# Optimization experiments

Hardware: AMD Instinct MI355X
Metric: run time of the kernel (lower is better)

## Reference

```python
import jax, jax.numpy as jnp
import numpy as np

CONTEXT_LENGTHS = [1, 3, 5, 7]
PADS = [(f - 1) // 2 for f in CONTEXT_LENGTHS]  # p(f) for odd f
B, H, L, DK = 2, 8, 1024, 64
C = H * DK  # conv channels = d_k * n_heads


def _conv1d(x, w, b, pad):
    # x: (b, C, L), w: (C, C, f), b: (C,) -- torch Conv1d semantics
    y = jax.lax.conv_general_dilated(
        x, w, window_strides=(1,), padding=[(pad, pad)],
        dimension_numbers=("NCH", "OIH", "NCH"))
    return y + b[None, :, None]


def _plane(a, w, b, pad, out_len):
    # Faithful to: conv(a.reshape(b, h*d_k, -1)).reshape(b, h, -1, d_k)[:, :, :out_len, :]
    bsz, h, l, d = a.shape
    y = _conv1d(a.reshape(bsz, h * d, l), w, b, pad)
    return y.reshape(bsz, h, -1, d)[:, :, :out_len, :]


def setup_inputs() -> dict:
    key = jax.random.key(0)
    ks = jax.random.split(key, 12)
    inp = {
        "Q": jax.random.normal(ks[0], (B, H, L, DK), jnp.float32),
        "K": jax.random.normal(ks[1], (B, H, L, DK), jnp.float32),
        "V": jax.random.normal(ks[2], (B, H, L, DK), jnp.float32),
        # causal mask: True = masked
        "attn_mask": jnp.broadcast_to(
            jnp.triu(jnp.ones((L, L), jnp.bool_), k=1), (B, H, L, L)),
    }
    for i, f in enumerate(CONTEXT_LENGTHS):
        scale = 1.0 / np.sqrt(C * f)
        inp[f"conv_w{i}"] = jax.random.normal(ks[3 + i], (C, C, f), jnp.float32) * scale
        inp[f"conv_b{i}"] = jax.random.normal(ks[7 + i], (C,), jnp.float32) * scale
    return inp


def reference(Q, K, V, attn_mask,
              conv_w0, conv_b0, conv_w1, conv_b1,
              conv_w2, conv_b2, conv_w3, conv_b3):
    ws = [conv_w0, conv_w1, conv_w2, conv_w3]
    bs = [conv_b0, conv_b1, conv_b2, conv_b3]
    b, h, l, d_k = Q.shape
    l_k = K.shape[2]
    p = len(CONTEXT_LENGTHS)
    Q_l = [_plane(Q, ws[i], bs[i], PADS[i], l) for i in range(p)]
    K_l = [_plane(K, ws[i], bs[i], PADS[i], l_k) for i in range(p)]
    # replicate torch.cat(dim=0).reshape(b, h, p, l, d) exactly (row-major)
    Q_p = jnp.concatenate(Q_l, axis=0).reshape(b, h, p, l, d_k)
    K_p = jnp.concatenate(K_l, axis=0).reshape(b, h, p, l_k, d_k)
    scores = jnp.einsum("bhpqd,bhpkd->bhpqk", Q_p, K_p) / np.sqrt(d_k).astype(np.float32)
    scores = jnp.where(attn_mask[:, :, None, :, :], jnp.float32(-1e9), scores)
    attn = jax.nn.softmax(scores, axis=-1)
    attn = jnp.max(attn, axis=2)  # max over planes -> (b,h,q,k)
    context = jnp.einsum("bhqk,bhkd->bhqd", attn, V)
    return (context, attn)
```

## Files before the change

### kernel.cpp

```cpp
#include <hip/hip_runtime.h>
#include <math.h>

#define C_CH 512
#define L_SEQ 1024
#define DK 64
#define NP 4
#define SC2 0.1803368801111f

typedef __attribute__((ext_vector_type(8))) short short8;
typedef __attribute__((ext_vector_type(4))) float f32x4;

__device__ __forceinline__ unsigned short f2bf(float f) {
    union { float f; unsigned u; } v; v.f = f;
    unsigned u = v.u;
    u += 0x7FFFu + ((u >> 16) & 1u);
    return (unsigned short)(u >> 16);
}

__device__ __forceinline__ void unpack_tile128(int G, int& qt8, int& kt) {
    int cum = 0;
    for (int q8 = 7; q8 >= 0; q8--) {
        int c = 2 * q8 + 2;
        if (G < cum + c) { qt8 = q8; kt = G - cum; return; }
        cum += c;
    }
    qt8 = 0; kt = 0;
}

__global__ __launch_bounds__(256)
void prep_w_kernel(const float* __restrict__ w0, const float* __restrict__ w1,
                   const float* __restrict__ w2, const float* __restrict__ w3,
                   unsigned short* __restrict__ Wb) {
    int tg = blockIdx.y;
    int plane, t;
    if (tg < 1)      { plane = 0; t = tg; }
    else if (tg < 4) { plane = 1; t = tg - 1; }
    else if (tg < 9) { plane = 2; t = tg - 4; }
    else             { plane = 3; t = tg - 9; }
    const float* W = (plane == 0) ? w0 : (plane == 1) ? w1 : (plane == 2) ? w2 : w3;
    const int f = (plane == 0) ? 1 : (plane == 1) ? 3 : (plane == 2) ? 5 : 7;

    int co = blockIdx.x * 32 + (threadIdx.x >> 3);
    int c8 = threadIdx.x & 7;
    for (int it = 0; it < 8; it++) {
        int ci = c8 * 8 + it * 64;
        unsigned short o[8];
#pragma unroll
        for (int jj = 0; jj < 8; jj++)
            o[jj] = f2bf(W[(size_t)(co * C_CH + ci + jj) * f + t]);
        *(short8*)&Wb[((size_t)tg * C_CH + co) * C_CH + ci] = *(short8*)o;
    }
}

__global__ __launch_bounds__(256)
void prep_x_kernel(const float* __restrict__ Qin, const float* __restrict__ Kin,
                   unsigned short* __restrict__ Xt) {
    int tb = blockIdx.z;
    int tensor = tb >> 1, b = tb & 1;
    const float* X = (tensor ? Kin : Qin) + (size_t)b * C_CH * L_SEQ;
    unsigned short* O = Xt + (size_t)tb * 1032 * C_CH;

    int pos0 = blockIdx.x * 64;
    int ci0  = blockIdx.y * 64;
    int tid = threadIdx.x;

    __shared__ float tile[64][65];
    int tx = tid & 15, ty = tid >> 4;
#pragma unroll
    for (int rr = 0; rr < 4; rr++) {
        int ci_l = ty + rr * 16;
        float4 v = *(const float4*)&X[(size_t)(ci0 + ci_l) * L_SEQ + pos0 + tx * 4];
        tile[tx * 4 + 0][ci_l] = v.x;
        tile[tx * 4 + 1][ci_l] = v.y;
        tile[tx * 4 + 2][ci_l] = v.z;
        tile[tx * 4 + 3][ci_l] = v.w;
    }
    __syncthreads();
#pragma unroll
    for (int pp = 0; pp < 2; pp++) {
        int pos_l = (tid >> 3) + pp * 32;
        int cg = (tid & 7) * 8;
        unsigned short o[8];
#pragma unroll
        for (int jj = 0; jj < 8; jj++) o[jj] = f2bf(tile[pos_l][cg + jj]);
        *(short8*)&O[(size_t)(pos0 + pos_l + 4) * C_CH + ci0 + cg] = *(short8*)o;
    }
    if (blockIdx.x == 0) {
        int r = tid >> 6, cc = tid & 63;
        O[(size_t)r * C_CH + ci0 + cc] = 0;
    }
    if (blockIdx.x == 15) {
        int r = tid >> 6, cc = tid & 63;
        O[(size_t)(1028 + r) * C_CH + ci0 + cc] = 0;
    }
}

__global__ __launch_bounds__(256)
void conv_mfma_kernel(const unsigned short* __restrict__ Xt,
                      const unsigned short* __restrict__ Wb,
                      const float* __restrict__ b0, const float* __restrict__ b1,
                      const float* __restrict__ b2, const float* __restrict__ b3,
                      unsigned short* __restrict__ Qp, unsigned short* __restrict__ Kp) {
    const int fs[4]   = {1, 3, 5, 7};
    const int toff[4] = {0, 1, 4, 9};
    int id = blockIdx.x;
    int plane, rel;
    if (id < 128)      { plane = 0; rel = id; }
    else if (id < 256) { plane = 1; rel = id - 128; }
    else if (id < 384) { plane = 3; rel = id - 256; }
    else               { plane = 2; rel = id - 384; }
    int co0  = (rel & 3) * 128;
    int pos0 = ((rel >> 2) & 7) * 128;
    int tb   = rel >> 5;
    int tensor = tb >> 1, b = tb & 1;
    const int f   = fs[plane];
    const int pad = (f - 1) >> 1;
    const int n   = f * 16;
    const float* bias = (plane == 0) ? b0 : (plane == 1) ? b1 : (plane == 2) ? b2 : b3;
    unsigned short* Out = tensor ? Kp : Qp;
    const unsigned short* Xbase = Xt + (size_t)tb * 1032 * C_CH;

    __shared__ __align__(16) unsigned short As[2][4096];
    __shared__ __align__(16) unsigned short Bs[2][4096];

    int tid  = threadIdx.x;
    int w    = tid >> 6;
    int lane = tid & 63;
    int l15  = lane & 15;
    int quad = lane >> 4;
    int wm = (w & 1) * 64;
    int wn = (w >> 1) * 64;
    int rowL = tid >> 2;
    int cS   = tid & 3;

    int woff[2];
#pragma unroll
    for (int rep = 0; rep < 2; rep++) {
        int r = rowL + rep * 64;
        int line = r >> 1;
        int sl = (((r & 1) << 2) | cS) ^ (line & 7);
        woff[rep] = line * 64 + sl * 8;
    }
    int aoff[4], boff[4];
#pragma unroll
    for (int mi = 0; mi < 4; mi++) {
        int r = wm + mi * 16 + l15;
        int line = r >> 1;
        aoff[mi] = line * 64 + ((((r & 1) << 2) | quad) ^ (line & 7)) * 8;
        int r2 = wn + mi * 16 + l15;
        int line2 = r2 >> 1;
        boff[mi] = line2 * 64 + ((((r2 & 1) << 2) | quad) ^ (line2 & 7)) * 8;
    }

    f32x4 acc[4][4];
#pragma unroll
    for (int mi = 0; mi < 4; mi++)
#pragma unroll
        for (int ni = 0; ni < 4; ni++) acc[mi][ni] = (f32x4){0.f, 0.f, 0.f, 0.f};

    short8 pA[2], pB[2];
    {
        const unsigned short* Wsl = Wb + ((size_t)toff[plane] * C_CH + co0) * C_CH;
        const unsigned short* Xsl = Xbase + (size_t)(pos0 - pad + 4) * C_CH;
#pragma unroll
        for (int rep = 0; rep < 2; rep++) {
            int r = rowL + rep * 64;
            pA[rep] = *(const short8*)&Wsl[(size_t)r * C_CH + cS * 8];
            pB[rep] = *(const short8*)&Xsl[(size_t)r * C_CH + cS * 8];
        }
    }

    for (int it = 0; it < n; it++) {
        int cur = it & 1;
        *(short8*)&As[cur][woff[0]] = pA[0];
        *(short8*)&As[cur][woff[1]] = pA[1];
        *(short8*)&Bs[cur][woff[0]] = pB[0];
        *(short8*)&Bs[cur][woff[1]] = pB[1];
        __syncthreads();

        if (it + 1 < n) {
            int t = (it + 1) >> 4, cc = (it + 1) & 15;
            const unsigned short* Wsl =
                Wb + ((size_t)(toff[plane] + t) * C_CH + co0) * C_CH + cc * 32;
            const unsigned short* Xsl =
                Xbase + (size_t)(pos0 + t - pad + 4) * C_CH + cc * 32;
#pragma unroll
            for (int rep = 0; rep < 2; rep++) {
                int r = rowL + rep * 64;
                pA[rep] = *(const short8*)&Wsl[(size_t)r * C_CH + cS * 8];
                pB[rep] = *(const short8*)&Xsl[(size_t)r * C_CH + cS * 8];
            }
        }

        short8 af[4], bf[4];
#pragma unroll
        for (int mi = 0; mi < 4; mi++) af[mi] = *(const short8*)&As[cur][aoff[mi]];
#pragma unroll
        for (int ni = 0; ni < 4; ni++) bf[ni] = *(const short8*)&Bs[cur][boff[ni]];
#pragma unroll
        for (int mi = 0; mi < 4; mi++)
#pragma unroll
            for (int ni = 0; ni < 4; ni++)
                acc[mi][ni] = __builtin_amdgcn_mfma_f32_16x16x32_bf16(
                    af[mi], bf[ni], acc[mi][ni], 0, 0, 0);
    }

#pragma unroll
    for (int mi = 0; mi < 4; mi++)
#pragma unroll
        for (int r = 0; r < 4; r++) {
            int co = co0 + wm + mi * 16 + quad * 4 + r;
            int h = co >> 6, cl = co & 63;
            float bv = bias[co];
            size_t sbase = (size_t)((b * 8 + h) * NP + plane) * L_SEQ * DK;
#pragma unroll
            for (int ni = 0; ni < 4; ni++) {
                int pos = pos0 + wn + ni * 16 + l15;
                int l = cl * 16 + (pos >> 6);
                int d = pos & 63;
                Out[sbase + (size_t)l * DK + d] = f2bf(acc[mi][ni][r] + bv);
            }
        }
}

__global__ __launch_bounds__(512)
void attn_stats_kernel(const unsigned short* __restrict__ Qb,
                       const unsigned short* __restrict__ Kb,
                       float* __restrict__ pl) {
    int qt8, kt;
    unpack_tile128(blockIdx.x, qt8, kt);
    int bh = blockIdx.y;
    int tid = threadIdx.x;
    int w = tid >> 6, lane = tid & 63, l15 = lane & 15, quad = lane >> 4;
    int q0 = qt8 * 128, k0 = kt * 64;
    int qrow0 = q0 + w * 16;

    if (qrow0 + 15 < k0) return;

    int b2 = bh >> 3, h2 = bh & 7;
    int plane  = b2 * 2 + (h2 >> 2);
    int b_orig = (h2 >> 1) & 1;
    int h_base = (h2 & 1) * 4;

    float l[NP][4];
#pragma unroll
    for (int p = 0; p < NP; p++)
        for (int r = 0; r < 4; r++) l[p][r] = 0.f;

#pragma unroll
    for (int p = 0; p < NP; p++) {
        size_t slice = (size_t)((b_orig * 8 + h_base + p) * NP + plane);
        const unsigned short* kb = Kb + slice * L_SEQ * DK;
        const unsigned short* qrow =
            Qb + (slice * L_SEQ + (size_t)(qrow0 + l15)) * DK + quad * 8;
        short8 qa0 = *(const short8*)(qrow);
        short8 qa1 = *(const short8*)(qrow + 32);

        f32x4 c[4];
#pragma unroll
        for (int s = 0; s < 4; s++) {
            const unsigned short* kr = kb + (size_t)(k0 + s * 16 + l15) * DK + quad * 8;
            short8 kb0 = *(const short8*)(kr);
            short8 kb1 = *(const short8*)(kr + 32);
            f32x4 acc = {0.f, 0.f, 0.f, 0.f};
            acc = __builtin_amdgcn_mfma_f32_16x16x32_bf16(qa0, kb0, acc, 0, 0, 0);
            acc = __builtin_amdgcn_mfma_f32_16x16x32_bf16(qa1, kb1, acc, 0, 0, 0);
            c[s] = acc;
        }
#pragma unroll
        for (int r = 0; r < 4; r++) {
            int qg = qrow0 + quad * 4 + r;
#pragma unroll
            for (int s = 0; s < 4; s++) {
                float x = c[s][r] * SC2;
                if (k0 + s * 16 + l15 > qg) x = -1e30f;
                l[p][r] += exp2f(x);
            }
        }
    }

    int qt64 = qt8 * 2 + (w >> 2);
    size_t base = ((size_t)(bh * 16 + qt64) * 16 + kt) * 256;
#pragma unroll
    for (int p = 0; p < NP; p++)
#pragma unroll
        for (int r = 0; r < 4; r++) {
            float ll = l[p][r];
            ll += __shfl_xor(ll, 1);
            ll += __shfl_xor(ll, 2);
            ll += __shfl_xor(ll, 4);
            ll += __shfl_xor(ll, 8);
            if (l15 == 0)
                pl[base + p * 64 + ((w & 3) * 16 + quad * 4 + r)] = ll;
        }
}

__global__ __launch_bounds__(256)
void attn_combine_kernel(const float* __restrict__ pl,
                         float* __restrict__ fstats,
                         float* __restrict__ out_attn) {
    int qt = blockIdx.x, bh = blockIdx.y;
    int tid = threadIdx.x;
    size_t sb = (size_t)(bh * 16 + qt) * 16 * 256;

    float l = 0.f;
    for (int kt = 0; kt <= qt; kt++)
        l += pl[sb + (size_t)kt * 256 + tid];
    fstats[(size_t)(bh * 16 + qt) * 256 + tid] = __log2f(l);

    int r = tid >> 2;
    float4 z = make_float4(0.f, 0.f, 0.f, 0.f);
    int kz = (qt + 1) * 64;
    size_t abase = ((size_t)bh * L_SEQ + qt * 64 + r) * L_SEQ;
    for (int k = kz + (tid & 3) * 4; k < L_SEQ; k += 16)
        *(float4*)&out_attn[abase + k] = z;
}

__global__ __launch_bounds__(512)
void attn_apply_kernel(const unsigned short* __restrict__ Qb,
                       const unsigned short* __restrict__ Kb,
                       const float* __restrict__ fstats,
                       float* __restrict__ out_attn) {
    int qt8, kt;
    unpack_tile128(blockIdx.x, qt8, kt);
    int bh = blockIdx.y;
    int tid = threadIdx.x;
    int w = tid >> 6, lane = tid & 63, l15 = lane & 15, quad = lane >> 4;
    int q0 = qt8 * 128, k0 = kt * 64;
    int qrow0 = q0 + w * 16;

    __shared__ float zsm[512];
    {
        int p = tid >> 7, row = tid & 127;
        int qt64 = qt8 * 2 + (row >> 6);
        zsm[tid] = fstats[(size_t)(bh * 16 + qt64) * 256 + p * 64 + (row & 63)];
    }
    __syncthreads();

    if (qrow0 + 15 < k0) {
#pragma unroll
        for (int s = 0; s < 4; s++)
#pragma unroll
            for (int r = 0; r < 4; r++) {
                int qg = qrow0 + quad * 4 + r;
                out_attn[((size_t)bh * L_SEQ + qg) * L_SEQ + k0 + s * 16 + l15] = 0.f;
            }
        return;
    }

    int b2 = bh >> 3, h2 = bh & 7;
    int plane  = b2 * 2 + (h2 >> 2);
    int b_orig = (h2 >> 1) & 1;
    int h_base = (h2 & 1) * 4;

    float run[4][4];
#pragma unroll
    for (int s = 0; s < 4; s++)
        for (int r = 0; r < 4; r++) run[s][r] = -1e30f;

#pragma unroll
    for (int p = 0; p < NP; p++) {
        size_t slice = (size_t)((b_orig * 8 + h_base + p) * NP + plane);
        const unsigned short* kb = Kb + slice * L_SEQ * DK;
        const unsigned short* qrow =
            Qb + (slice * L_SEQ + (size_t)(qrow0 + l15)) * DK + quad * 8;
        short8 qa0 = *(const short8*)(qrow);
        short8 qa1 = *(const short8*)(qrow + 32);

        f32x4 c[4];
#pragma unroll
        for (int s = 0; s < 4; s++) {
            const unsigned short* kr = kb + (size_t)(k0 + s * 16 + l15) * DK + quad * 8;
            short8 kb0 = *(const short8*)(kr);
            short8 kb1 = *(const short8*)(kr + 32);
            f32x4 acc = {0.f, 0.f, 0.f, 0.f};
            acc = __builtin_amdgcn_mfma_f32_16x16x32_bf16(qa0, kb0, acc, 0, 0, 0);
            acc = __builtin_amdgcn_mfma_f32_16x16x32_bf16(qa1, kb1, acc, 0, 0, 0);
            c[s] = acc;
        }
#pragma unroll
        for (int r = 0; r < 4; r++) {
            float zp = zsm[p * 128 + (w * 16 + quad * 4 + r)];
#pragma unroll
            for (int s = 0; s < 4; s++)
                run[s][r] = fmaxf(run[s][r], c[s][r] * SC2 - zp);
        }
    }

#pragma unroll
    for (int s = 0; s < 4; s++)
#pragma unroll
        for (int r = 0; r < 4; r++) {
            int qg = qrow0 + quad * 4 + r;
            int kg = k0 + s * 16 + l15;
            float a = (kg > qg) ? 0.f : exp2f(run[s][r]);
            out_attn[((size_t)bh * L_SEQ + qg) * L_SEQ + kg] = a;
        }
}

__global__ __launch_bounds__(512)
void ctx_gemm_kernel(const float* __restrict__ attn, const float* __restrict__ V,
                     float* __restrict__ out_ctx) {
    int qt = 15 - blockIdx.x;
    int bh = blockIdx.y;
    int tid = threadIdx.x;
    int w = tid >> 6, lane = tid & 63, l15 = lane & 15, quad = lane >> 4;
    int q0 = qt * 64;
    int nk = (qt + 1) * 64;
    int wq = (w & 3) * 16;
    int ds0 = (w >> 2) * 2;

    __shared__ __align__(16) unsigned short vts[64 * 136];

    const float* Arow = attn + ((size_t)bh * L_SEQ + q0 + wq + l15) * L_SEQ;
    const float* Vb = V + (size_t)bh * L_SEQ * DK;

    f32x4 acc[2];
    acc[0] = (f32x4){0.f, 0.f, 0.f, 0.f};
    acc[1] = (f32x4){0.f, 0.f, 0.f, 0.f};

    for (int c0 = 0; c0 < nk; c0 += 128) {
        int rem = min(128, nk - c0);
        __syncthreads();
        {
            int kl = tid >> 2, db = (tid & 3) * 16;
            if (kl < rem) {
                const float* vr = Vb + (size_t)(c0 + kl) * DK + db;
                float vv[16];
                *(float4*)&vv[0]  = *(const float4*)(vr);
                *(float4*)&vv[4]  = *(const float4*)(vr + 4);
                *(float4*)&vv[8]  = *(const float4*)(vr + 8);
                *(float4*)&vv[12] = *(const float4*)(vr + 12);
#pragma unroll
                for (int jj = 0; jj < 16; jj++)
                    vts[(db + jj) * 136 + kl] = f2bf(vv[jj]);
            }
        }
        __syncthreads();

        int nss = rem >> 5;
        for (int ss = 0; ss < nss; ss++) {
            int kk = c0 + ss * 32 + quad * 8;
            float4 a0 = *(const float4*)&Arow[kk];
            float4 a1 = *(const float4*)&Arow[kk + 4];
            unsigned short af[8];
            af[0] = f2bf(a0.x); af[1] = f2bf(a0.y); af[2] = f2bf(a0.z); af[3] = f2bf(a0.w);
            af[4] = f2bf(a1.x); af[5] = f2bf(a1.y); af[6] = f2bf(a1.z); af[7] = f2bf(a1.w);
            short8 afv = *(short8*)af;
#pragma unroll
            for (int t = 0; t < 2; t++) {
                short8 bf = *(const short8*)&vts[((ds0 + t) * 16 + l15) * 136 +
                                                 ss * 32 + quad * 8];
                acc[t] = __builtin_amdgcn_mfma_f32_16x16x32_bf16(afv, bf, acc[t], 0, 0, 0);
            }
        }
    }

#pragma unroll
    for (int t = 0; t < 2; t++)
#pragma unroll
        for (int r = 0; r < 4; r++) {
            int qg = q0 + wq + quad * 4 + r;
            out_ctx[((size_t)bh * L_SEQ + qg) * DK + (ds0 + t) * 16 + l15] = acc[t][r];
        }
}

extern "C" void kernel_launch(void* const* d_in, const int* in_sizes, int n_in,
                              void* d_out, int out_size, void* d_ws, size_t ws_size,
                              hipStream_t stream) {
    const float* Q  = (const float*)d_in[0];
    const float* K  = (const float*)d_in[1];
    const float* V  = (const float*)d_in[2];
    const float* w0 = (const float*)d_in[4];
    const float* b0 = (const float*)d_in[5];
    const float* w1 = (const float*)d_in[6];
    const float* b1 = (const float*)d_in[7];
    const float* w2 = (const float*)d_in[8];
    const float* b2 = (const float*)d_in[9];
    const float* w3 = (const float*)d_in[10];
    const float* b3 = (const float*)d_in[11];

    char* ws = (char*)d_ws;
    unsigned short* Wb = (unsigned short*)(ws);
    unsigned short* Xt = (unsigned short*)(ws + 8388608);
    unsigned short* Qp = (unsigned short*)(ws + 12615680);
    unsigned short* Kp = (unsigned short*)(ws + 21004288);
    float* pl     = (float*)(ws);
    float* fstats = (float*)(ws + 4194304);

    float* out_ctx  = (float*)d_out;
    float* out_attn = out_ctx + 1048576;

    prep_w_kernel<<<dim3(16, 16), 256, 0, stream>>>(w0, w1, w2, w3, Wb);
    prep_x_kernel<<<dim3(16, 8, 4), 256, 0, stream>>>(Q, K, Xt);
    conv_mfma_kernel<<<dim3(512), 256, 0, stream>>>(Xt, Wb, b0, b1, b2, b3, Qp, Kp);
    attn_stats_kernel<<<dim3(72, 16), 512, 0, stream>>>(Qp, Kp, pl);
    attn_combine_kernel<<<dim3(16, 16), 256, 0, stream>>>(pl, fstats, out_attn);
    attn_apply_kernel<<<dim3(72, 16), 512, 0, stream>>>(Qp, Kp, fstats, out_attn);
    ctx_gemm_kernel<<<dim3(16, 16), 512, 0, stream>>>(out_attn, V, out_ctx);
}
```

Measured before the change: 374.0 us.

## Retile conv, fold combine into apply, split-K the context GEMM with reduction

```diff
diff --git a/kernel.cpp b/kernel.cpp
--- a/kernel.cpp
+++ b/kernel.cpp
@@ -25,6 +25,22 @@
         cum += c;
     }
     qt8 = 0; kt = 0;
+}
+
+__device__ __forceinline__ void unpack_group(int G, int& qt, int& kt0, int& kt1,
+                                             int& j, int& ng) {
+    int q = 15, cum = 0, jj = 0;
+    for (; q >= 0; q--) {
+        int g = (q + 4) >> 2;
+        if (G < cum + g) { jj = G - cum; break; }
+        cum += g;
+    }
+    qt = q;
+    ng = (q + 4) >> 2;
+    j = jj;
+    int n = q + 1;
+    kt0 = (jj * n) / ng;
+    kt1 = ((jj + 1) * n) / ng;
 }
 
 __global__ __launch_bounds__(256)
@@ -104,14 +120,11 @@
     const int fs[4]   = {1, 3, 5, 7};
     const int toff[4] = {0, 1, 4, 9};
     int id = blockIdx.x;
-    int plane, rel;
-    if (id < 128)      { plane = 0; rel = id; }
-    else if (id < 256) { plane = 1; rel = id - 128; }
-    else if (id < 384) { plane = 3; rel = id - 256; }
-    else               { plane = 2; rel = id - 384; }
+    int plane = (id < 256) ? 0 : (id < 512) ? 1 : (id < 768) ? 3 : 2;
+    int rel = id & 255;
     int co0  = (rel & 3) * 128;
-    int pos0 = ((rel >> 2) & 7) * 128;
-    int tb   = rel >> 5;
+    int pos0 = ((rel >> 2) & 15) * 64;
+    int tb   = rel >> 6;
     int tensor = tb >> 1, b = tb & 1;
     const int f   = fs[plane];
     const int pad = (f - 1) >> 1;
@@ -121,7 +134,7 @@
     const unsigned short* Xbase = Xt + (size_t)tb * 1032 * C_CH;
 
     __shared__ __align__(16) unsigned short As[2][4096];
-    __shared__ __align__(16) unsigned short Bs[2][4096];
+    __shared__ __align__(16) unsigned short Bs[2][2048];
 
     int tid  = threadIdx.x;
     int w    = tid >> 6;
@@ -129,53 +142,54 @@
     int l15  = lane & 15;
     int quad = lane >> 4;
     int wm = (w & 1) * 64;
-    int wn = (w >> 1) * 64;
-    int rowL = tid >> 2;
-    int cS   = tid & 3;
-
-    int woff[2];
+    int wn = (w >> 1) * 32;
+
+    int rA0 = tid >> 2, sA = tid & 3;
+    int woffA[2], woffB;
 #pragma unroll
     for (int rep = 0; rep < 2; rep++) {
-        int r = rowL + rep * 64;
+        int r = rA0 + rep * 64;
         int line = r >> 1;
-        int sl = (((r & 1) << 2) | cS) ^ (line & 7);
-        woff[rep] = line * 64 + sl * 8;
-    }
-    int aoff[4], boff[4];
+        woffA[rep] = line * 64 + (((((r & 1) << 2) | sA)) ^ (line & 7)) * 8;
+    }
+    {
+        int line = rA0 >> 1;
+        woffB = line * 64 + (((((rA0 & 1) << 2) | sA)) ^ (line & 7)) * 8;
+    }
+    int aoff[4], boff[2];
 #pragma unroll
     for (int mi = 0; mi < 4; mi++) {
         int r = wm + mi * 16 + l15;
         int line = r >> 1;
         aoff[mi] = line * 64 + ((((r & 1) << 2) | quad) ^ (line & 7)) * 8;
-        int r2 = wn + mi * 16 + l15;
-        int line2 = r2 >> 1;
-        boff[mi] = line2 * 64 + ((((r2 & 1) << 2) | quad) ^ (line2 & 7)) * 8;
-    }
-
-    f32x4 acc[4][4];
+    }
+#pragma unroll
+    for (int ni = 0; ni < 2; ni++) {
+        int r = wn + ni * 16 + l15;
+        int line = r >> 1;
+        boff[ni] = line * 64 + ((((r & 1) << 2) | quad) ^ (line & 7)) * 8;
+    }
+
+    f32x4 acc[4][2];
 #pragma unroll
     for (int mi = 0; mi < 4; mi++)
 #pragma unroll
-        for (int ni = 0; ni < 4; ni++) acc[mi][ni] = (f32x4){0.f, 0.f, 0.f, 0.f};
-
-    short8 pA[2], pB[2];
+        for (int ni = 0; ni < 2; ni++) acc[mi][ni] = (f32x4){0.f, 0.f, 0.f, 0.f};
+
+    short8 pA[2], pB;
     {
         const unsigned short* Wsl = Wb + ((size_t)toff[plane] * C_CH + co0) * C_CH;
         const unsigned short* Xsl = Xbase + (size_t)(pos0 - pad + 4) * C_CH;
-#pragma unroll
-        for (int rep = 0; rep < 2; rep++) {
-            int r = rowL + rep * 64;
-            pA[rep] = *(const short8*)&Wsl[(size_t)r * C_CH + cS * 8];
-            pB[rep] = *(const short8*)&Xsl[(size_t)r * C_CH + cS * 8];
-        }
+        pA[0] = *(const short8*)&Wsl[(size_t)rA0 * C_CH + sA * 8];
+        pA[1] = *(const short8*)&Wsl[(size_t)(rA0 + 64) * C_CH + sA * 8];
+        pB    = *(const short8*)&Xsl[(size_t)rA0 * C_CH + sA * 8];
     }
 
     for (int it = 0; it < n; it++) {
         int cur = it & 1;
-        *(short8*)&As[cur][woff[0]] = pA[0];
-        *(short8*)&As[cur][woff[1]] = pA[1];
-        *(short8*)&Bs[cur][woff[0]] = pB[0];
-        *(short8*)&Bs[cur][woff[1]] = pB[1];
+        *(short8*)&As[cur][woffA[0]] = pA[0];
+        *(short8*)&As[cur][woffA[1]] = pA[1];
+        *(short8*)&Bs[cur][woffB]    = pB;
         __syncthreads();
 
         if (it + 1 < n) {
@@ -184,43 +198,49 @@
                 Wb + ((size_t)(toff[plane] + t) * C_CH + co0) * C_CH + cc * 32;
             const unsigned short* Xsl =
                 Xbase + (size_t)(pos0 + t - pad + 4) * C_CH + cc * 32;
-#pragma unroll
-            for (int rep = 0; rep < 2; rep++) {
-                int r = rowL + rep * 64;
-                pA[rep] = *(const short8*)&Wsl[(size_t)r * C_CH + cS * 8];
-                pB[rep] = *(const short8*)&Xsl[(size_t)r * C_CH + cS * 8];
-            }
-        }
-
-        short8 af[4], bf[4];
+            pA[0] = *(const short8*)&Wsl[(size_t)rA0 * C_CH + sA * 8];
+            pA[1] = *(const short8*)&Wsl[(size_t)(rA0 + 64) * C_CH + sA * 8];
+            pB    = *(const short8*)&Xsl[(size_t)rA0 * C_CH + sA * 8];
+        }
+
+        short8 af[4], bf[2];
 #pragma unroll
         for (int mi = 0; mi < 4; mi++) af[mi] = *(const short8*)&As[cur][aoff[mi]];
 #pragma unroll
-        for (int ni = 0; ni < 4; ni++) bf[ni] = *(const short8*)&Bs[cur][boff[ni]];
+        for (int ni = 0; ni < 2; ni++) bf[ni] = *(const short8*)&Bs[cur][boff[ni]];
 #pragma unroll
         for (int mi = 0; mi < 4; mi++)
 #pragma unroll
-            for (int ni = 0; ni < 4; ni++)
+            for (int ni = 0; ni < 2; ni++)
                 acc[mi][ni] = __builtin_amdgcn_mfma_f32_16x16x32_bf16(
                     af[mi], bf[ni], acc[mi][ni], 0, 0, 0);
     }
 
+    __syncthreads();
+    unsigned short* Cs = &As[0][0];
 #pragma unroll
     for (int mi = 0; mi < 4; mi++)
 #pragma unroll
         for (int r = 0; r < 4; r++) {
-            int co = co0 + wm + mi * 16 + quad * 4 + r;
-            int h = co >> 6, cl = co & 63;
-            float bv = bias[co];
-            size_t sbase = (size_t)((b * 8 + h) * NP + plane) * L_SEQ * DK;
-#pragma unroll
-            for (int ni = 0; ni < 4; ni++) {
-                int pos = pos0 + wn + ni * 16 + l15;
-                int l = cl * 16 + (pos >> 6);
-                int d = pos & 63;
-                Out[sbase + (size_t)l * DK + d] = f2bf(acc[mi][ni][r] + bv);
-            }
-        }
+            int co_l = wm + mi * 16 + quad * 4 + r;
+            float bv = bias[co0 + co_l];
+#pragma unroll
+            for (int ni = 0; ni < 2; ni++)
+                Cs[co_l * 64 + wn + ni * 16 + l15] = f2bf(acc[mi][ni][r] + bv);
+        }
+    __syncthreads();
+    {
+        int co_l = tid >> 1, half = tid & 1;
+        int co = co0 + co_l;
+        int h = co >> 6, cl = co & 63;
+        int l = cl * 16 + (pos0 >> 6);
+        size_t obase =
+            ((size_t)((b * 8 + h) * NP + plane) * L_SEQ + l) * DK + half * 32;
+#pragma unroll
+        for (int k = 0; k < 4; k++)
+            *(short8*)&Out[obase + k * 8] =
+                *(const short8*)&Cs[co_l * 64 + half * 32 + k * 8];
+    }
 }
 
 __global__ __launch_bounds__(512)
@@ -295,37 +315,38 @@
         }
 }
 
-__global__ __launch_bounds__(256)
-void attn_combine_kernel(const float* __restrict__ pl,
-                         float* __restrict__ fstats,
-                         float* __restrict__ out_attn) {
-    int qt = blockIdx.x, bh = blockIdx.y;
-    int tid = threadIdx.x;
-    size_t sb = (size_t)(bh * 16 + qt) * 16 * 256;
-
-    float l = 0.f;
-    for (int kt = 0; kt <= qt; kt++)
-        l += pl[sb + (size_t)kt * 256 + tid];
-    fstats[(size_t)(bh * 16 + qt) * 256 + tid] = __log2f(l);
-
-    int r = tid >> 2;
-    float4 z = make_float4(0.f, 0.f, 0.f, 0.f);
-    int kz = (qt + 1) * 64;
-    size_t abase = ((size_t)bh * L_SEQ + qt * 64 + r) * L_SEQ;
-    for (int k = kz + (tid & 3) * 4; k < L_SEQ; k += 16)
-        *(float4*)&out_attn[abase + k] = z;
-}
-
 __global__ __launch_bounds__(512)
 void attn_apply_kernel(const unsigned short* __restrict__ Qb,
                        const unsigned short* __restrict__ Kb,
-                       const float* __restrict__ fstats,
+                       const float* __restrict__ pl,
                        float* __restrict__ out_attn) {
-    int qt8, kt;
-    unpack_tile128(blockIdx.x, qt8, kt);
+    int G = blockIdx.x;
     int bh = blockIdx.y;
     int tid = threadIdx.x;
     int w = tid >> 6, lane = tid & 63, l15 = lane & 15, quad = lane >> 4;
+
+    int qt8, kt;
+    if (G >= 72) {
+        int z = G - 72, cum = 0;
+        qt8 = 0; kt = 0;
+        for (int q8 = 0; q8 < 8; q8++) {
+            int c = 14 - 2 * q8;
+            if (z < cum + c) { qt8 = q8; kt = 2 * q8 + 2 + (z - cum); break; }
+            cum += c;
+        }
+        int q0 = qt8 * 128, k0 = kt * 64;
+        int qrow0 = q0 + w * 16;
+#pragma unroll
+        for (int s = 0; s < 4; s++)
+#pragma unroll
+            for (int r = 0; r < 4; r++) {
+                int qg = qrow0 + quad * 4 + r;
+                out_attn[((size_t)bh * L_SEQ + qg) * L_SEQ + k0 + s * 16 + l15] = 0.f;
+            }
+        return;
+    }
+
+    unpack_tile128(G, qt8, kt);
     int q0 = qt8 * 128, k0 = kt * 64;
     int qrow0 = q0 + w * 16;
 
@@ -333,7 +354,11 @@
     {
         int p = tid >> 7, row = tid & 127;
         int qt64 = qt8 * 2 + (row >> 6);
-        zsm[tid] = fstats[(size_t)(bh * 16 + qt64) * 256 + p * 64 + (row & 63)];
+        size_t sb = (size_t)(bh * 16 + qt64) * 16 * 256 + p * 64 + (row & 63);
+        float lsum = 0.f;
+        for (int kt2 = 0; kt2 <= qt64; kt2++)
+            lsum += pl[sb + (size_t)kt2 * 256];
+        zsm[tid] = __log2f(lsum);
     }
     __syncthreads();
 
@@ -398,71 +423,102 @@
         }
 }
 
-__global__ __launch_bounds__(512)
+__global__ __launch_bounds__(256)
 void ctx_gemm_kernel(const float* __restrict__ attn, const float* __restrict__ V,
-                     float* __restrict__ out_ctx) {
-    int qt = 15 - blockIdx.x;
+                     float* __restrict__ pctx) {
+    int qt, kt0, kt1, j, ng;
+    unpack_group(blockIdx.x, qt, kt0, kt1, j, ng);
     int bh = blockIdx.y;
     int tid = threadIdx.x;
     int w = tid >> 6, lane = tid & 63, l15 = lane & 15, quad = lane >> 4;
     int q0 = qt * 64;
-    int nk = (qt + 1) * 64;
-    int wq = (w & 3) * 16;
-    int ds0 = (w >> 2) * 2;
-
-    __shared__ __align__(16) unsigned short vts[64 * 136];
-
-    const float* Arow = attn + ((size_t)bh * L_SEQ + q0 + wq + l15) * L_SEQ;
+
+    __shared__ __align__(16) unsigned short vts[2][64 * 80];
+
+    const float* Arow = attn + ((size_t)bh * L_SEQ + q0 + w * 16 + l15) * L_SEQ;
     const float* Vb = V + (size_t)bh * L_SEQ * DK;
 
-    f32x4 acc[2];
-    acc[0] = (f32x4){0.f, 0.f, 0.f, 0.f};
-    acc[1] = (f32x4){0.f, 0.f, 0.f, 0.f};
-
-    for (int c0 = 0; c0 < nk; c0 += 128) {
-        int rem = min(128, nk - c0);
-        __syncthreads();
+    f32x4 acc[4];
+#pragma unroll
+    for (int ds = 0; ds < 4; ds++) acc[ds] = (f32x4){0.f, 0.f, 0.f, 0.f};
+
+    for (int kt = kt0; kt < kt1; kt++) {
+        int k0 = kt * 64;
+        unsigned short* vb = vts[kt & 1];
         {
             int kl = tid >> 2, db = (tid & 3) * 16;
-            if (kl < rem) {
-                const float* vr = Vb + (size_t)(c0 + kl) * DK + db;
-                float vv[16];
-                *(float4*)&vv[0]  = *(const float4*)(vr);
-                *(float4*)&vv[4]  = *(const float4*)(vr + 4);
-                *(float4*)&vv[8]  = *(const float4*)(vr + 8);
-                *(float4*)&vv[12] = *(const float4*)(vr + 12);
-#pragma unroll
-                for (int jj = 0; jj < 16; jj++)
-                    vts[(db + jj) * 136 + kl] = f2bf(vv[jj]);
-            }
+            const float* vr = Vb + (size_t)(k0 + kl) * DK + db;
+            float vv[16];
+            *(float4*)&vv[0]  = *(const float4*)(vr);
+            *(float4*)&vv[4]  = *(const float4*)(vr + 4);
+            *(float4*)&vv[8]  = *(const float4*)(vr + 8);
+            *(float4*)&vv[12] = *(const float4*)(vr + 12);
+#pragma unroll
+            for (int jj = 0; jj < 16; jj++)
+                vb[(db + jj) * 80 + kl] = f2bf(vv[jj]);
         }
         __syncthreads();
 
-        int nss = rem >> 5;
-        for (int ss = 0; ss < nss; ss++) {
-            int kk = c0 + ss * 32 + quad * 8;
-            float4 a0 = *(const float4*)&Arow[kk];
-            float4 a1 = *(const float4*)&Arow[kk + 4];
-            unsigned short af[8];
-            af[0] = f2bf(a0.x); af[1] = f2bf(a0.y); af[2] = f2bf(a0.z); af[3] = f2bf(a0.w);
-            af[4] = f2bf(a1.x); af[5] = f2bf(a1.y); af[6] = f2bf(a1.z); af[7] = f2bf(a1.w);
-            short8 afv = *(short8*)af;
-#pragma unroll
-            for (int t = 0; t < 2; t++) {
-                short8 bf = *(const short8*)&vts[((ds0 + t) * 16 + l15) * 136 +
-                                                 ss * 32 + quad * 8];
-                acc[t] = __builtin_amdgcn_mfma_f32_16x16x32_bf16(afv, bf, acc[t], 0, 0, 0);
-            }
-        }
-    }
-
-#pragma unroll
-    for (int t = 0; t < 2; t++)
+        int kk = k0 + quad * 8;
+        float4 a0 = *(const float4*)&Arow[kk];
+        float4 a1 = *(const float4*)&Arow[kk + 4];
+        float4 a2 = *(const float4*)&Arow[kk + 32];
+        float4 a3 = *(const float4*)&Arow[kk + 36];
+        unsigned short af[16];
+        af[0] = f2bf(a0.x); af[1] = f2bf(a0.y); af[2] = f2bf(a0.z); af[3] = f2bf(a0.w);
+        af[4] = f2bf(a1.x); af[5] = f2bf(a1.y); af[6] = f2bf(a1.z); af[7] = f2bf(a1.w);
+        af[8]  = f2bf(a2.x); af[9]  = f2bf(a2.y); af[10] = f2bf(a2.z); af[11] = f2bf(a2.w);
+        af[12] = f2bf(a3.x); af[13] = f2bf(a3.y); af[14] = f2bf(a3.z); af[15] = f2bf(a3.w);
+        short8 af0 = *(short8*)&af[0];
+        short8 af1 = *(short8*)&af[8];
+#pragma unroll
+        for (int ds = 0; ds < 4; ds++) {
+            short8 bf0 = *(const short8*)&vb[(ds * 16 + l15) * 80 + quad * 8];
+            short8 bf1 = *(const short8*)&vb[(ds * 16 + l15) * 80 + 32 + quad * 8];
+            acc[ds] = __builtin_amdgcn_mfma_f32_16x16x32_bf16(af0, bf0, acc[ds], 0, 0, 0);
+            acc[ds] = __builtin_amdgcn_mfma_f32_16x16x32_bf16(af1, bf1, acc[ds], 0, 0, 0);
+        }
+    }
+
+    size_t pbase = ((size_t)(bh * 16 + qt) * 4 + j) * 4096;
+#pragma unroll
+    for (int ds = 0; ds < 4; ds++)
 #pragma unroll
         for (int r = 0; r < 4; r++) {
-            int qg = q0 + wq + quad * 4 + r;
-            out_ctx[((size_t)bh * L_SEQ + qg) * DK + (ds0 + t) * 16 + l15] = acc[t][r];
-        }
+            int qloc = w * 16 + quad * 4 + r;
+            pctx[pbase + (size_t)qloc * 64 + ds * 16 + l15] = acc[ds][r];
+        }
+}
+
+__global__ __launch_bounds__(256)
+void ctx_reduce_kernel(const float* __restrict__ pctx, float* __restrict__ out_ctx) {
+    int qt = blockIdx.x, bh = blockIdx.y;
+    int tid = threadIdx.x;
+    int ng = (qt + 4) >> 2;
+    size_t base = (size_t)(bh * 16 + qt) * 4 * 4096;
+    int row = tid >> 2, c = (tid & 3) * 16;
+    size_t off = (size_t)row * 64 + c;
+
+    float4 a0 = *(const float4*)&pctx[base + off];
+    float4 a1 = *(const float4*)&pctx[base + off + 4];
+    float4 a2 = *(const float4*)&pctx[base + off + 8];
+    float4 a3 = *(const float4*)&pctx[base + off + 12];
+    for (int g = 1; g < ng; g++) {
+        size_t gb = base + (size_t)g * 4096 + off;
+        float4 b0 = *(const float4*)&pctx[gb];
+        float4 b1 = *(const float4*)&pctx[gb + 4];
+        float4 b2 = *(const float4*)&pctx[gb + 8];
+        float4 b3 = *(const float4*)&pctx[gb + 12];
+        a0.x += b0.x; a0.y += b0.y; a0.z += b0.z; a0.w += b0.w;
+        a1.x += b1.x; a1.y += b1.y; a1.z += b1.z; a1.w += b1.w;
+        a2.x += b2.x; a2.y += b2.y; a2.z += b2.z; a2.w += b2.w;
+        a3.x += b3.x; a3.y += b3.y; a3.z += b3.z; a3.w += b3.w;
+    }
+    size_t ob = ((size_t)bh * L_SEQ + qt * 64 + row) * DK + c;
+    *(float4*)&out_ctx[ob]      = a0;
+    *(float4*)&out_ctx[ob + 4]  = a1;
+    *(float4*)&out_ctx[ob + 8]  = a2;
+    *(float4*)&out_ctx[ob + 12] = a3;
 }
 
 extern "C" void kernel_launch(void* const* d_in, const int* in_sizes, int n_in,
@@ -485,17 +541,17 @@
     unsigned short* Xt = (unsigned short*)(ws + 8388608);
     unsigned short* Qp = (unsigned short*)(ws + 12615680);
     unsigned short* Kp = (unsigned short*)(ws + 21004288);
-    float* pl     = (float*)(ws);
-    float* fstats = (float*)(ws + 4194304);
+    float* pctx        = (float*)(ws + 29392896);
+    float* pl = (float*)(ws);
 
     float* out_ctx  = (float*)d_out;
     float* out_attn = out_ctx + 1048576;
 
     prep_w_kernel<<<dim3(16, 16), 256, 0, stream>>>(w0, w1, w2, w3, Wb);
     prep_x_kernel<<<dim3(16, 8, 4), 256, 0, stream>>>(Q, K, Xt);
-    conv_mfma_kernel<<<dim3(512), 256, 0, stream>>>(Xt, Wb, b0, b1, b2, b3, Qp, Kp);
+    conv_mfma_kernel<<<dim3(1024), 256, 0, stream>>>(Xt, Wb, b0, b1, b2, b3, Qp, Kp);
     attn_stats_kernel<<<dim3(72, 16), 512, 0, stream>>>(Qp, Kp, pl);
-    attn_combine_kernel<<<dim3(16, 16), 256, 0, stream>>>(pl, fstats, out_attn);
-    attn_apply_kernel<<<dim3(72, 16), 512, 0, stream>>>(Qp, Kp, fstats, out_attn);
-    ctx_gemm_kernel<<<dim3(16, 16), 512, 0, stream>>>(out_attn, V, out_ctx);
-}
+    attn_apply_kernel<<<dim3(128, 16), 512, 0, stream>>>(Qp, Kp, pl, out_attn);
+    ctx_gemm_kernel<<<dim3(40, 16), 256, 0, stream>>>(out_attn, V, pctx);
+    ctx_reduce_kernel<<<dim3(16, 16), 256, 0, stream>>>(pctx, out_ctx);
+}
```

Measured after the change: 359.2 us. 1.04x faster.
